# Kernel tuning notes

Measured on AMD Instinct MI355X. Metric: run time of the kernel, lower is better.

## Reference

```python
import jax, jax.numpy as jnp
import numpy as np

INT8_MAX = 127.0
EQN = 'bsd,df->bsf'


def _quantize(x, axes):
    """Symmetric int8 abs-max quantization over contraction axes.

    Returns (q, scale) with q in [-127, 127] (stored fp32) and scale shaped
    with keepdims so that q * scale ~ x.
    """
    absmax = jnp.max(jnp.abs(x), axis=axes, keepdims=True)
    scale = absmax / INT8_MAX
    scale = jnp.where(scale == 0.0, jnp.ones_like(scale), scale)
    q = jnp.clip(jnp.round(x / scale), -INT8_MAX, INT8_MAX)
    return q, scale


def setup_inputs() -> dict:
    key = jax.random.key(0)
    k1, k2 = jax.random.split(key)
    lhs = jax.random.normal(k1, (4, 2048, 4096), dtype=jnp.float32)
    rhs = jax.random.normal(k2, (4096, 16384), dtype=jnp.float32)
    return {"lhs": lhs, "rhs": rhs}


def reference(lhs, rhs):
    # AQT quantized einsum 'bsd,df->bsf':
    #   per-(b,s)-row int8 quantization of lhs over contraction axis d,
    #   per-column (f) int8 quantization of rhs over contraction axis d,
    #   low-precision matmul, then dequantize by the outer product of scales.
    q_lhs, s_lhs = _quantize(lhs, axes=(2,))   # q:[b,s,d], s:[b,s,1]
    q_rhs, s_rhs = _quantize(rhs, axes=(0,))   # q:[d,f],  s:[1,f]
    acc = jnp.einsum(EQN, q_lhs, q_rhs)        # int-valued accumulation in fp32
    # dequant: scales factor out of the contraction
    return acc * s_lhs * s_rhs[None]           # [b,s,f]
```

## Files before the change

kernel.cpp:

```cpp
#include <hip/hip_runtime.h>
#include <hip/hip_bf16.h>
#include <stdint.h>

#define M_TOT 8192
#define N_TOT 16384
#define K_TOT 4096

typedef int v4i __attribute__((ext_vector_type(4)));
typedef int v16i __attribute__((ext_vector_type(16)));

__device__ __forceinline__ float fix_scale(float s) { return s == 0.0f ? 1.0f : s; }

__device__ __forceinline__ void gload_lds16(const void* g, void* l) {
    __builtin_amdgcn_global_load_lds((__attribute__((address_space(1))) void*)g,
                                     (__attribute__((address_space(3))) void*)l,
                                     16, 0, 0);
}

__device__ __forceinline__ int8_t quant1(float x, float scale) {
    float r = fminf(127.0f, fmaxf(-127.0f, rintf(x / scale)));
    return (int8_t)(int)r;
}

__device__ __forceinline__ unsigned pack4(float4 v, float scale) {
    unsigned b0 = (unsigned char)quant1(v.x, scale);
    unsigned b1 = (unsigned char)quant1(v.y, scale);
    unsigned b2 = (unsigned char)quant1(v.z, scale);
    unsigned b3 = (unsigned char)quant1(v.w, scale);
    return b0 | (b1 << 8) | (b2 << 16) | (b3 << 24);
}


__global__ __launch_bounds__(256) void k_quant_lhs(const float* __restrict__ x,
                                                   int8_t* __restrict__ qt,
                                                   float* __restrict__ s) {
    const int row = blockIdx.x;
    const int t = threadIdx.x;
    const float4* xr = (const float4*)(x + (size_t)row * K_TOT);
    float4 v[4];
    float m = 0.0f;
#pragma unroll
    for (int i = 0; i < 4; ++i) {
        v[i] = xr[t * 4 + i];
        m = fmaxf(m, fmaxf(fmaxf(fabsf(v[i].x), fabsf(v[i].y)),
                           fmaxf(fabsf(v[i].z), fabsf(v[i].w))));
    }
#pragma unroll
    for (int off = 32; off; off >>= 1) m = fmaxf(m, __shfl_xor(m, off));
    __shared__ float wmax[4];
    if ((t & 63) == 0) wmax[t >> 6] = m;
    __syncthreads();
    m = fmaxf(fmaxf(wmax[0], wmax[1]), fmaxf(wmax[2], wmax[3]));
    const float scale = fix_scale(m / 127.0f);
    if (t == 0) s[row] = scale;

    v4i w;
#pragma unroll
    for (int i = 0; i < 4; ++i) w[i] = (int)pack4(v[i], scale);

    const int mt = row >> 8, mb = (row >> 5) & 7, r = row & 31;
    const int kt = t >> 2, s2 = (t >> 1) & 1, h = t & 1;
    const size_t gidx = (size_t)(mt * 64 + kt) * 1024 + (size_t)((mb * 2 + s2) * 64 + h * 32 + r);
    ((v4i*)qt)[gidx] = w;
}

__global__ __launch_bounds__(256) void k_rhs_absmax(const float* __restrict__ rhs,
                                                    unsigned* __restrict__ amax) {
    const int f = blockIdx.x * 256 + threadIdx.x;
    const int d0 = blockIdx.y * 256;
    const float* p = rhs + (size_t)d0 * N_TOT + f;
    float m = 0.0f;
#pragma unroll 4
    for (int d = 0; d < 256; ++d)
        m = fmaxf(m, fabsf(p[(size_t)d * N_TOT]));
    atomicMax(amax + f, __float_as_uint(m));
}

__global__ __launch_bounds__(256) void k_rhs_scale(const unsigned* __restrict__ amax,
                                                   float* __restrict__ s) {
    const int f = blockIdx.x * 256 + threadIdx.x;
    s[f] = fix_scale(__uint_as_float(amax[f]) / 127.0f);
}

__global__ __launch_bounds__(256) void k_quant_rhs_t(const float* __restrict__ rhs,
                                                     const float* __restrict__ s,
                                                     int8_t* __restrict__ qt) {
    const int f0 = blockIdx.x * 64;
    const int d0 = blockIdx.y * 64;
    const int t = threadIdx.x;
    __shared__ float sc[64];
    __shared__ alignas(16) int8_t tile[64][64];
    if (t < 64) sc[t] = s[f0 + t];
    __syncthreads();
    const int fl = (t & 15) * 4;
    const int rl = t >> 4;
#pragma unroll
    for (int i = 0; i < 4; ++i) {
        const int dl = i * 16 + rl;
        float4 v = *(const float4*)(rhs + (size_t)(d0 + dl) * N_TOT + f0 + fl);
        tile[fl + 0][dl] = quant1(v.x, sc[fl + 0]);
        tile[fl + 1][dl] = quant1(v.y, sc[fl + 1]);
        tile[fl + 2][dl] = quant1(v.z, sc[fl + 2]);
        tile[fl + 3][dl] = quant1(v.w, sc[fl + 3]);
    }
    __syncthreads();
    const int nb_l = t >> 7, s2 = (t >> 6) & 1, h = (t >> 5) & 1, r = t & 31;
    const int col_local = nb_l * 32 + r;
    const int kb16 = s2 * 2 + h;
    const int nt = f0 >> 8;
    const int nb = ((f0 >> 5) & 7) + nb_l;
    const int kt = d0 >> 6;
    const size_t gidx = (size_t)(nt * 64 + kt) * 1024 + (size_t)((nb * 2 + s2) * 64 + h * 32 + r);
    ((v4i*)qt)[gidx] = *(const v4i*)&tile[col_local][kb16 * 16];
}

#define BM 256
#define BN 256
#define BK 64
#define NKT (K_TOT / BK)

#define MFMA_I8(A, B, Cc) __builtin_amdgcn_mfma_i32_32x32x32_i8((A), (B), (Cc), 0, 0, 0)

__global__ __launch_bounds__(512, 2) void k_gemm(const int8_t* __restrict__ qA,
                                                 const int8_t* __restrict__ qB,
                                                 const float* __restrict__ sA,
                                                 const float* __restrict__ sB,
                                                 float* __restrict__ C) {
    __shared__ alignas(1024) int8_t lds[3][32768];

    const int bid = blockIdx.x;
    const int scc = bid >> 6;
    const int ii = bid & 63;
    const int mt = ii & 31;
    const int ntile = (scc << 1) | (ii >> 5);
    const int bm0 = mt << 8;
    const int bn0 = ntile << 8;

    const int tid = threadIdx.x;
    const int wave = tid >> 6;
    const int lane = tid & 63;
    const int wm = (wave >> 2) * 128;
    const int wn = (wave & 3) * 64;

    const int8_t* aBase = qA + (size_t)mt * (64 * 16384);
    const int8_t* bBase = qB + (size_t)ntile * (64 * 16384);

    const int aoff = (wave >> 2) * 8192 + lane * 16;
    const int boff = 16384 + (wave & 3) * 4096 + lane * 16;

    v16i acc[4][2];
#pragma unroll
    for (int f = 0; f < 4; ++f)
#pragma unroll
        for (int n = 0; n < 2; ++n)
#pragma unroll
            for (int e = 0; e < 16; ++e) acc[f][n][e] = 0;

    auto stage_half = [&](int kt, int h) {
        const int b = kt % 3;
        const int loff = h * 8192 + tid * 16;
        const int8_t* src = (h < 2) ? (aBase + (size_t)kt * 16384 + h * 8192 + tid * 16)
                                    : (bBase + (size_t)kt * 16384 + (h - 2) * 8192 + tid * 16);
        gload_lds16(src, &lds[b][loff]);
    };

    stage_half(0, 0); stage_half(0, 1); stage_half(0, 2); stage_half(0, 3);
    stage_half(1, 0); stage_half(1, 1); stage_half(1, 2); stage_half(1, 3);
    asm volatile("s_waitcnt vmcnt(4)" ::: "memory");
    __builtin_amdgcn_s_barrier();

    for (int kt = 0; kt < NKT; ++kt) {
        const int8_t* a = &lds[kt % 3][0];
        const bool st = (kt + 2 < NKT);
        v4i af[4], bf[2];

        af[0] = *(const v4i*)(a + aoff + 0 * 2048);
        af[1] = *(const v4i*)(a + aoff + 1 * 2048);
        af[2] = *(const v4i*)(a + aoff + 2 * 2048);
        af[3] = *(const v4i*)(a + aoff + 3 * 2048);
        bf[0] = *(const v4i*)(a + boff + 0 * 2048);
        bf[1] = *(const v4i*)(a + boff + 1 * 2048);
        if (st) { stage_half(kt + 2, 0); stage_half(kt + 2, 1); }
        __builtin_amdgcn_s_barrier();
        asm volatile("s_waitcnt lgkmcnt(0)" ::: "memory");
        __builtin_amdgcn_s_setprio(1);
        acc[0][0] = MFMA_I8(af[0], bf[0], acc[0][0]);
        acc[0][1] = MFMA_I8(af[0], bf[1], acc[0][1]);
        acc[1][0] = MFMA_I8(af[1], bf[0], acc[1][0]);
        acc[1][1] = MFMA_I8(af[1], bf[1], acc[1][1]);
        acc[2][0] = MFMA_I8(af[2], bf[0], acc[2][0]);
        acc[2][1] = MFMA_I8(af[2], bf[1], acc[2][1]);
        acc[3][0] = MFMA_I8(af[3], bf[0], acc[3][0]);
        acc[3][1] = MFMA_I8(af[3], bf[1], acc[3][1]);
        __builtin_amdgcn_s_setprio(0);
        __builtin_amdgcn_s_barrier();

        af[0] = *(const v4i*)(a + aoff + 0 * 2048 + 1024);
        af[1] = *(const v4i*)(a + aoff + 1 * 2048 + 1024);
        af[2] = *(const v4i*)(a + aoff + 2 * 2048 + 1024);
        af[3] = *(const v4i*)(a + aoff + 3 * 2048 + 1024);
        bf[0] = *(const v4i*)(a + boff + 0 * 2048 + 1024);
        bf[1] = *(const v4i*)(a + boff + 1 * 2048 + 1024);
        if (st) { stage_half(kt + 2, 2); stage_half(kt + 2, 3); }
        __builtin_amdgcn_s_barrier();
        asm volatile("s_waitcnt lgkmcnt(0)" ::: "memory");
        __builtin_amdgcn_s_setprio(1);
        acc[0][0] = MFMA_I8(af[0], bf[0], acc[0][0]);
        acc[0][1] = MFMA_I8(af[0], bf[1], acc[0][1]);
        acc[1][0] = MFMA_I8(af[1], bf[0], acc[1][0]);
        acc[1][1] = MFMA_I8(af[1], bf[1], acc[1][1]);
        acc[2][0] = MFMA_I8(af[2], bf[0], acc[2][0]);
        acc[2][1] = MFMA_I8(af[2], bf[1], acc[2][1]);
        acc[3][0] = MFMA_I8(af[3], bf[0], acc[3][0]);
        acc[3][1] = MFMA_I8(af[3], bf[1], acc[3][1]);
        __builtin_amdgcn_s_setprio(0);
        if (kt + 2 < NKT)      asm volatile("s_waitcnt vmcnt(4)" ::: "memory");
        else if (kt + 1 < NKT) asm volatile("s_waitcnt vmcnt(0)" ::: "memory");
        __builtin_amdgcn_s_barrier();
    }

    const int cc0 = lane & 31;
    const int rbase = (lane >> 5) * 4;
#pragma unroll
    for (int f = 0; f < 4; ++f) {
#pragma unroll
        for (int r = 0; r < 16; ++r) {
            const int gr = bm0 + wm + f * 32 + (r & 3) + 8 * (r >> 2) + rbase;
            const float sa = sA[gr];
            float* crow = C + (size_t)gr * N_TOT + bn0 + wn;
#pragma unroll
            for (int n = 0; n < 2; ++n)
                crow[n * 32 + cc0] = (float)acc[f][n][r] * sa * sB[bn0 + wn + n * 32 + cc0];
        }
    }
}

extern "C" void kernel_launch(void* const* d_in, const int* in_sizes, int n_in,
                              void* d_out, int out_size, void* d_ws, size_t ws_size,
                              hipStream_t stream) {
    const float* lhs = (const float*)d_in[0];
    const float* rhs = (const float*)d_in[1];
    float* out = (float*)d_out;
    char* ws = (char*)d_ws;

    int8_t* qA = (int8_t*)ws;
    int8_t* qB = (int8_t*)(ws + (size_t)33554432);
    float* sA = (float*)(ws + (size_t)33554432 + 67108864);
    float* sB = sA + M_TOT;
    unsigned* amax = (unsigned*)(sB + N_TOT);

    hipMemsetAsync(amax, 0, N_TOT * sizeof(unsigned), stream);

    k_quant_lhs<<<M_TOT, 256, 0, stream>>>(lhs, qA, sA);
    k_rhs_absmax<<<dim3(N_TOT / 256, K_TOT / 256), 256, 0, stream>>>(rhs, amax);
    k_rhs_scale<<<N_TOT / 256, 256, 0, stream>>>(amax, sB);
    k_quant_rhs_t<<<dim3(N_TOT / 64, K_TOT / 64), 256, 0, stream>>>(rhs, sB, qB);
    k_gemm<<<(M_TOT / BM) * (N_TOT / BN), 512, 0, stream>>>(qA, qB, sA, sB, out);
}
```

Before: 744.7 us.

## Deepen LDS ring to four stages and double-buffer MFMA fragments in registers

Result: slower. 762.0 us (+2.3%).

```diff
diff --git a/kernel.cpp b/kernel.cpp
--- a/kernel.cpp
+++ b/kernel.cpp
@@ -121,12 +121,17 @@
 
 #define MFMA_I8(A, B, Cc) __builtin_amdgcn_mfma_i32_32x32x32_i8((A), (B), (Cc), 0, 0, 0)
 
+struct Frags {
+    v4i a0[4], a1[4];
+    v4i b0[2], b1[2];
+};
+
 __global__ __launch_bounds__(512, 2) void k_gemm(const int8_t* __restrict__ qA,
                                                  const int8_t* __restrict__ qB,
                                                  const float* __restrict__ sA,
                                                  const float* __restrict__ sB,
                                                  float* __restrict__ C) {
-    __shared__ alignas(1024) int8_t lds[3][32768];
+    __shared__ alignas(1024) int8_t lds[4][32768];
 
     const int bid = blockIdx.x;
     const int scc = bid >> 6;
@@ -156,67 +161,85 @@
 #pragma unroll
             for (int e = 0; e < 16; ++e) acc[f][n][e] = 0;
 
-    auto stage_half = [&](int kt, int h) {
-        const int b = kt % 3;
-        const int loff = h * 8192 + tid * 16;
-        const int8_t* src = (h < 2) ? (aBase + (size_t)kt * 16384 + h * 8192 + tid * 16)
-                                    : (bBase + (size_t)kt * 16384 + (h - 2) * 8192 + tid * 16);
-        gload_lds16(src, &lds[b][loff]);
+    auto stage_kt = [&](int kt) {
+        const int b = kt & 3;
+#pragma unroll
+        for (int h = 0; h < 4; ++h) {
+            const int loff = h * 8192 + tid * 16;
+            const int8_t* src = (h < 2) ? (aBase + (size_t)kt * 16384 + h * 8192 + tid * 16)
+                                        : (bBase + (size_t)kt * 16384 + (h - 2) * 8192 + tid * 16);
+            gload_lds16(src, &lds[b][loff]);
+        }
     };
 
-    stage_half(0, 0); stage_half(0, 1); stage_half(0, 2); stage_half(0, 3);
-    stage_half(1, 0); stage_half(1, 1); stage_half(1, 2); stage_half(1, 3);
+    stage_kt(0); stage_kt(1); stage_kt(2);
     asm volatile("s_waitcnt vmcnt(4)" ::: "memory");
     __builtin_amdgcn_s_barrier();
 
-    for (int kt = 0; kt < NKT; ++kt) {
-        const int8_t* a = &lds[kt % 3][0];
-        const bool st = (kt + 2 < NKT);
-        v4i af[4], bf[2];
-
-        af[0] = *(const v4i*)(a + aoff + 0 * 2048);
-        af[1] = *(const v4i*)(a + aoff + 1 * 2048);
-        af[2] = *(const v4i*)(a + aoff + 2 * 2048);
-        af[3] = *(const v4i*)(a + aoff + 3 * 2048);
-        bf[0] = *(const v4i*)(a + boff + 0 * 2048);
-        bf[1] = *(const v4i*)(a + boff + 1 * 2048);
-        if (st) { stage_half(kt + 2, 0); stage_half(kt + 2, 1); }
-        __builtin_amdgcn_s_barrier();
-        asm volatile("s_waitcnt lgkmcnt(0)" ::: "memory");
+    Frags F0, F1;
+    {
+        const int8_t* nb = &lds[0][0];
+#pragma unroll
+        for (int f = 0; f < 4; ++f) {
+            F0.a0[f] = *(const v4i*)(nb + aoff + f * 2048);
+            F0.a1[f] = *(const v4i*)(nb + aoff + f * 2048 + 1024);
+        }
+#pragma unroll
+        for (int n = 0; n < 2; ++n) {
+            F0.b0[n] = *(const v4i*)(nb + boff + n * 2048);
+            F0.b1[n] = *(const v4i*)(nb + boff + n * 2048 + 1024);
+        }
+    }
+
+    auto body = [&](int kt, Frags& cur, Frags& nxt) {
+        const bool rd = (kt + 1 < NKT);
+        const bool st = (kt + 3 < NKT);
+        const int8_t* nb = &lds[(kt + 1) & 3][0];
+
+        if (rd) {
+#pragma unroll
+            for (int f = 0; f < 4; ++f) nxt.a0[f] = *(const v4i*)(nb + aoff + f * 2048);
+#pragma unroll
+            for (int n = 0; n < 2; ++n) nxt.b0[n] = *(const v4i*)(nb + boff + n * 2048);
+        }
+        if (st) stage_kt(kt + 3);
+        __builtin_amdgcn_sched_barrier(0);
+
         __builtin_amdgcn_s_setprio(1);
-        acc[0][0] = MFMA_I8(af[0], bf[0], acc[0][0]);
-        acc[0][1] = MFMA_I8(af[0], bf[1], acc[0][1]);
-        acc[1][0] = MFMA_I8(af[1], bf[0], acc[1][0]);
-        acc[1][1] = MFMA_I8(af[1], bf[1], acc[1][1]);
-        acc[2][0] = MFMA_I8(af[2], bf[0], acc[2][0]);
-        acc[2][1] = MFMA_I8(af[2], bf[1], acc[2][1]);
-        acc[3][0] = MFMA_I8(af[3], bf[0], acc[3][0]);
-        acc[3][1] = MFMA_I8(af[3], bf[1], acc[3][1]);
+#pragma unroll
+        for (int f = 0; f < 4; ++f) {
+            acc[f][0] = MFMA_I8(cur.a0[f], cur.b0[0], acc[f][0]);
+            acc[f][1] = MFMA_I8(cur.a0[f], cur.b0[1], acc[f][1]);
+        }
         __builtin_amdgcn_s_setprio(0);
-        __builtin_amdgcn_s_barrier();
-
-        af[0] = *(const v4i*)(a + aoff + 0 * 2048 + 1024);
-        af[1] = *(const v4i*)(a + aoff + 1 * 2048 + 1024);
-        af[2] = *(const v4i*)(a + aoff + 2 * 2048 + 1024);
-        af[3] = *(const v4i*)(a + aoff + 3 * 2048 + 1024);
-        bf[0] = *(const v4i*)(a + boff + 0 * 2048 + 1024);
-        bf[1] = *(const v4i*)(a + boff + 1 * 2048 + 1024);
-        if (st) { stage_half(kt + 2, 2); stage_half(kt + 2, 3); }
-        __builtin_amdgcn_s_barrier();
-        asm volatile("s_waitcnt lgkmcnt(0)" ::: "memory");
+
+        if (rd) {
+#pragma unroll
+            for (int f = 0; f < 4; ++f) nxt.a1[f] = *(const v4i*)(nb + aoff + f * 2048 + 1024);
+#pragma unroll
+            for (int n = 0; n < 2; ++n) nxt.b1[n] = *(const v4i*)(nb + boff + n * 2048 + 1024);
+        }
+        __builtin_amdgcn_sched_barrier(0);
+
         __builtin_amdgcn_s_setprio(1);
-        acc[0][0] = MFMA_I8(af[0], bf[0], acc[0][0]);
-        acc[0][1] = MFMA_I8(af[0], bf[1], acc[0][1]);
-        acc[1][0] = MFMA_I8(af[1], bf[0], acc[1][0]);
-        acc[1][1] = MFMA_I8(af[1], bf[1], acc[1][1]);
-        acc[2][0] = MFMA_I8(af[2], bf[0], acc[2][0]);
-        acc[2][1] = MFMA_I8(af[2], bf[1], acc[2][1]);
-        acc[3][0] = MFMA_I8(af[3], bf[0], acc[3][0]);
-        acc[3][1] = MFMA_I8(af[3], bf[1], acc[3][1]);
+#pragma unroll
+        for (int f = 0; f < 4; ++f) {
+            acc[f][0] = MFMA_I8(cur.a1[f], cur.b1[0], acc[f][0]);
+            acc[f][1] = MFMA_I8(cur.a1[f], cur.b1[1], acc[f][1]);
+        }
         __builtin_amdgcn_s_setprio(0);
-        if (kt + 2 < NKT)      asm volatile("s_waitcnt vmcnt(4)" ::: "memory");
-        else if (kt + 1 < NKT) asm volatile("s_waitcnt vmcnt(0)" ::: "memory");
-        __builtin_amdgcn_s_barrier();
+
+        if (rd) {
+            asm volatile("s_waitcnt lgkmcnt(0)" ::: "memory");
+            if (st)                asm volatile("s_waitcnt vmcnt(4)" ::: "memory");
+            else if (kt + 2 < NKT) asm volatile("s_waitcnt vmcnt(0)" ::: "memory");
+            __builtin_amdgcn_s_barrier();
+        }
+    };
+
+    for (int kt = 0; kt < NKT; kt += 2) {
+        body(kt, F0, F1);
+        body(kt + 1, F1, F0);
     }
 
     const int cc0 = lane & 31;
```

## Use four waves per GEMM block with 128x128 warp tiles

Applied to the files above, without the earlier changes.

Result: no change. 751.2 us (+0.9%).

```diff
diff --git a/kernel.cpp b/kernel.cpp
--- a/kernel.cpp
+++ b/kernel.cpp
@@ -121,7 +121,7 @@
 
 #define MFMA_I8(A, B, Cc) __builtin_amdgcn_mfma_i32_32x32x32_i8((A), (B), (Cc), 0, 0, 0)
 
-__global__ __launch_bounds__(512, 2) void k_gemm(const int8_t* __restrict__ qA,
+__global__ __launch_bounds__(256, 1) void k_gemm(const int8_t* __restrict__ qA,
                                                  const int8_t* __restrict__ qB,
                                                  const float* __restrict__ sA,
                                                  const float* __restrict__ sB,
@@ -139,40 +139,42 @@
     const int tid = threadIdx.x;
     const int wave = tid >> 6;
     const int lane = tid & 63;
-    const int wm = (wave >> 2) * 128;
-    const int wn = (wave & 3) * 64;
+    const int wm = (wave >> 1) * 128;
+    const int wn = (wave & 1) * 128;
 
     const int8_t* aBase = qA + (size_t)mt * (64 * 16384);
     const int8_t* bBase = qB + (size_t)ntile * (64 * 16384);
 
-    const int aoff = (wave >> 2) * 8192 + lane * 16;
-    const int boff = 16384 + (wave & 3) * 4096 + lane * 16;
-
-    v16i acc[4][2];
+    const int aoff = (wave >> 1) * 8192 + lane * 16;
+    const int boff = 16384 + (wave & 1) * 8192 + lane * 16;
+
+    v16i acc[4][4];
 #pragma unroll
     for (int f = 0; f < 4; ++f)
 #pragma unroll
-        for (int n = 0; n < 2; ++n)
+        for (int n = 0; n < 4; ++n)
 #pragma unroll
             for (int e = 0; e < 16; ++e) acc[f][n][e] = 0;
 
-    auto stage_half = [&](int kt, int h) {
+    auto stage_half = [&](int kt, int half) {
         const int b = kt % 3;
-        const int loff = h * 8192 + tid * 16;
-        const int8_t* src = (h < 2) ? (aBase + (size_t)kt * 16384 + h * 8192 + tid * 16)
-                                    : (bBase + (size_t)kt * 16384 + (h - 2) * 8192 + tid * 16);
-        gload_lds16(src, &lds[b][loff]);
+        const int8_t* src = (half == 0) ? (aBase + (size_t)kt * 16384)
+                                        : (bBase + (size_t)kt * 16384);
+        const int loff = half * 16384;
+#pragma unroll
+        for (int h = 0; h < 4; ++h)
+            gload_lds16(src + h * 4096 + tid * 16, &lds[b][loff + h * 4096 + tid * 16]);
     };
 
-    stage_half(0, 0); stage_half(0, 1); stage_half(0, 2); stage_half(0, 3);
-    stage_half(1, 0); stage_half(1, 1); stage_half(1, 2); stage_half(1, 3);
-    asm volatile("s_waitcnt vmcnt(4)" ::: "memory");
+    stage_half(0, 0); stage_half(0, 1);
+    stage_half(1, 0); stage_half(1, 1);
+    asm volatile("s_waitcnt vmcnt(8)" ::: "memory");
     __builtin_amdgcn_s_barrier();
 
     for (int kt = 0; kt < NKT; ++kt) {
         const int8_t* a = &lds[kt % 3][0];
         const bool st = (kt + 2 < NKT);
-        v4i af[4], bf[2];
+        v4i af[4], bf[4];
 
         af[0] = *(const v4i*)(a + aoff + 0 * 2048);
         af[1] = *(const v4i*)(a + aoff + 1 * 2048);
@@ -180,18 +182,19 @@
         af[3] = *(const v4i*)(a + aoff + 3 * 2048);
         bf[0] = *(const v4i*)(a + boff + 0 * 2048);
         bf[1] = *(const v4i*)(a + boff + 1 * 2048);
-        if (st) { stage_half(kt + 2, 0); stage_half(kt + 2, 1); }
+        bf[2] = *(const v4i*)(a + boff + 2 * 2048);
+        bf[3] = *(const v4i*)(a + boff + 3 * 2048);
+        if (st) stage_half(kt + 2, 0);
         __builtin_amdgcn_s_barrier();
         asm volatile("s_waitcnt lgkmcnt(0)" ::: "memory");
         __builtin_amdgcn_s_setprio(1);
-        acc[0][0] = MFMA_I8(af[0], bf[0], acc[0][0]);
-        acc[0][1] = MFMA_I8(af[0], bf[1], acc[0][1]);
-        acc[1][0] = MFMA_I8(af[1], bf[0], acc[1][0]);
-        acc[1][1] = MFMA_I8(af[1], bf[1], acc[1][1]);
-        acc[2][0] = MFMA_I8(af[2], bf[0], acc[2][0]);
-        acc[2][1] = MFMA_I8(af[2], bf[1], acc[2][1]);
-        acc[3][0] = MFMA_I8(af[3], bf[0], acc[3][0]);
-        acc[3][1] = MFMA_I8(af[3], bf[1], acc[3][1]);
+#pragma unroll
+        for (int f = 0; f < 4; ++f) {
+            acc[f][0] = MFMA_I8(af[f], bf[0], acc[f][0]);
+            acc[f][1] = MFMA_I8(af[f], bf[1], acc[f][1]);
+            acc[f][2] = MFMA_I8(af[f], bf[2], acc[f][2]);
+            acc[f][3] = MFMA_I8(af[f], bf[3], acc[f][3]);
+        }
         __builtin_amdgcn_s_setprio(0);
         __builtin_amdgcn_s_barrier();
 
@@ -201,20 +204,21 @@
         af[3] = *(const v4i*)(a + aoff + 3 * 2048 + 1024);
         bf[0] = *(const v4i*)(a + boff + 0 * 2048 + 1024);
         bf[1] = *(const v4i*)(a + boff + 1 * 2048 + 1024);
-        if (st) { stage_half(kt + 2, 2); stage_half(kt + 2, 3); }
+        bf[2] = *(const v4i*)(a + boff + 2 * 2048 + 1024);
+        bf[3] = *(const v4i*)(a + boff + 3 * 2048 + 1024);
+        if (st) stage_half(kt + 2, 1);
         __builtin_amdgcn_s_barrier();
         asm volatile("s_waitcnt lgkmcnt(0)" ::: "memory");
         __builtin_amdgcn_s_setprio(1);
-        acc[0][0] = MFMA_I8(af[0], bf[0], acc[0][0]);
-        acc[0][1] = MFMA_I8(af[0], bf[1], acc[0][1]);
-        acc[1][0] = MFMA_I8(af[1], bf[0], acc[1][0]);
-        acc[1][1] = MFMA_I8(af[1], bf[1], acc[1][1]);
-        acc[2][0] = MFMA_I8(af[2], bf[0], acc[2][0]);
-        acc[2][1] = MFMA_I8(af[2], bf[1], acc[2][1]);
-        acc[3][0] = MFMA_I8(af[3], bf[0], acc[3][0]);
-        acc[3][1] = MFMA_I8(af[3], bf[1], acc[3][1]);
+#pragma unroll
+        for (int f = 0; f < 4; ++f) {
+            acc[f][0] = MFMA_I8(af[f], bf[0], acc[f][0]);
+            acc[f][1] = MFMA_I8(af[f], bf[1], acc[f][1]);
+            acc[f][2] = MFMA_I8(af[f], bf[2], acc[f][2]);
+            acc[f][3] = MFMA_I8(af[f], bf[3], acc[f][3]);
+        }
         __builtin_amdgcn_s_setprio(0);
-        if (kt + 2 < NKT)      asm volatile("s_waitcnt vmcnt(4)" ::: "memory");
+        if (kt + 2 < NKT)      asm volatile("s_waitcnt vmcnt(8)" ::: "memory");
         else if (kt + 1 < NKT) asm volatile("s_waitcnt vmcnt(0)" ::: "memory");
         __builtin_amdgcn_s_barrier();
     }
@@ -229,7 +233,7 @@
             const float sa = sA[gr];
             float* crow = C + (size_t)gr * N_TOT + bn0 + wn;
 #pragma unroll
-            for (int n = 0; n < 2; ++n)
+            for (int n = 0; n < 4; ++n)
                 crow[n * 32 + cc0] = (float)acc[f][n][r] * sa * sB[bn0 + wn + n * 32 + cc0];
         }
     }
@@ -255,5 +259,5 @@
     k_rhs_absmax<<<dim3(N_TOT / 256, K_TOT / 256), 256, 0, stream>>>(rhs, amax);
     k_rhs_scale<<<N_TOT / 256, 256, 0, stream>>>(amax, sB);
     k_quant_rhs_t<<<dim3(N_TOT / 64, K_TOT / 64), 256, 0, stream>>>(rhs, sB, qB);
-    k_gemm<<<(M_TOT / BM) * (N_TOT / BN), 512, 0, stream>>>(qA, qB, sA, sB, out);
-}
+    k_gemm<<<(M_TOT / BM) * (N_TOT / BN), 256, 0, stream>>>(qA, qB, sA, sB, out);
+}
```
